# Optimization experiments

Hardware: AMD Instinct MI355X
Metric: run time of the kernel (lower is better)

The kernel has to match this reference:

```python
import jax, jax.numpy as jnp
import numpy as np

B, S, D, H = 8, 1024, 1024, 16
HD = D // H  # head_dim = 64
SCALE = HD ** -0.5


def setup_inputs() -> dict:
    key = jax.random.key(0)
    ks = jax.random.split(key, 10)
    std = D ** -0.5
    return {
        "hidden_states": jax.random.normal(ks[0], (B, S, D), jnp.float32),
        "attn_mask": jnp.zeros((B, 1, S, S), jnp.float32),
        "prev_attn_weights": jax.random.normal(ks[1], (B, H, S, S), jnp.float32),
        "Wq": jax.random.normal(ks[2], (D, D), jnp.float32) * std,
        "bq": jnp.zeros((D,), jnp.float32),
        "Wk": jax.random.normal(ks[3], (D, D), jnp.float32) * std,
        "bk": jnp.zeros((D,), jnp.float32),
        "Wv": jax.random.normal(ks[4], (D, D), jnp.float32) * std,
        "bv": jnp.zeros((D,), jnp.float32),
    }


def _split_heads(x):
    # (B, S, D) -> (B, H, S, HD)
    return x.reshape(B, S, H, HD).transpose(0, 2, 1, 3)


def reference(hidden_states, attn_mask, prev_attn_weights, Wq, bq, Wk, bk, Wv, bv):
    q = _split_heads(hidden_states @ Wq + bq)
    k = _split_heads(hidden_states @ Wk + bk)
    v = _split_heads(hidden_states @ Wv + bv)
    # scaled dot-product scores + additive mask + realformer residual scores
    scores = jnp.einsum("bhqd,bhkd->bhqk", q, k) * SCALE
    scores = scores + attn_mask + prev_attn_weights
    probs = jax.nn.softmax(scores, axis=-1)  # dropout p=0 (eval)
    ctx = jnp.einsum("bhqk,bhkd->bhqd", probs, v)
    # (B, H, S, HD) -> (B, S, D)
    out = ctx.transpose(0, 2, 1, 3).reshape(B, S, D)
    return out
```

## Files before the change

kernel.cpp:

```cpp
#include <hip/hip_runtime.h>

#define B_  8
#define S_  1024
#define D_  1024
#define H_  16
#define HD_ 64
#define M_  8192
#define LOG2E 1.44269504088896f
#define QSCALE_ (0.125f * 1.44269504088896f)
#define MSHIFT_ 20.0f

typedef __attribute__((ext_vector_type(8))) short bf16x8;
typedef __attribute__((ext_vector_type(4))) float f32x4;

__device__ __forceinline__ unsigned short f2b(float x) {
  union { float f; unsigned u; } un; un.f = x;
  unsigned r = un.u + 0x7FFFu + ((un.u >> 16) & 1u);
  return (unsigned short)(r >> 16);
}

__global__ __launch_bounds__(256) void k_convert_x(const float* __restrict__ x,
                                                   unsigned short* __restrict__ o) {
  int i = (blockIdx.x * 256 + threadIdx.x) * 4;
  const int n = M_ * D_;
  const int stride = gridDim.x * 256 * 4;
  for (; i < n; i += stride) {
    const float4 v = *(const float4*)(x + i);
    ushort4 r;
    r.x = f2b(v.x); r.y = f2b(v.y); r.z = f2b(v.z); r.w = f2b(v.w);
    *(ushort4*)(o + i) = r;
  }
}

__global__ __launch_bounds__(256) void k_transpose_w(const float* __restrict__ Wq,
    const float* __restrict__ Wk, const float* __restrict__ Wv,
    unsigned short* __restrict__ Wt) {
  __shared__ float t[64][65];
  const float* W = (blockIdx.z == 0) ? Wq : ((blockIdx.z == 1) ? Wk : Wv);
  unsigned short* dst = Wt + (size_t)blockIdx.z * (D_ * D_);
  const int k0 = blockIdx.x * 64, n0 = blockIdx.y * 64;
  const int tid = threadIdx.x;
#pragma unroll
  for (int i = 0; i < 16; ++i) {
    const int lin = i * 256 + tid;
    const int r = lin >> 6, c = lin & 63;
    t[r][c] = W[(size_t)(k0 + r) * D_ + n0 + c];
  }
  __syncthreads();
#pragma unroll
  for (int i = 0; i < 16; ++i) {
    const int lin = i * 256 + tid;
    const int r = lin >> 6, c = lin & 63;
    dst[(size_t)(n0 + r) * D_ + k0 + c] = f2b(t[c][r]);
  }
}

template <int MODE>
__global__ __launch_bounds__(256) void k_proj(const unsigned short* __restrict__ X,
    const unsigned short* __restrict__ Wt,
    const float* __restrict__ bq, const float* __restrict__ bk, const float* __restrict__ bv,
    unsigned short* __restrict__ Qw, unsigned short* __restrict__ Kw,
    unsigned short* __restrict__ Vt) {
  __shared__ unsigned short xs[128 * 32];
  __shared__ unsigned short wsh[128 * 32];
  const int tid = threadIdx.x;
  const int lane = tid & 63, wv = tid >> 6;
  const int g = lane >> 4, li = lane & 15;
  const int m0 = blockIdx.x * 128;
  const int n0 = blockIdx.y * 128;
  const int wr = wv >> 1, wc = wv & 1;
  const int wtrow0 = (MODE == 0) ? n0 : (2048 + n0);

  f32x4 acc[4][4];
#pragma unroll
  for (int i = 0; i < 4; ++i)
#pragma unroll
    for (int j = 0; j < 4; ++j) acc[i][j] = (f32x4){0.f, 0.f, 0.f, 0.f};

  const int srow = wv * 32 + (lane >> 2);
  const int skel = (lane & 3) * 8;

  for (int k0 = 0; k0 < D_; k0 += 32) {
#pragma unroll
    for (int i = 0; i < 2; ++i) {
      const unsigned short* gx = X + (size_t)(m0 + srow + i * 16) * D_ + k0 + skel;
      const unsigned short* gw = Wt + (size_t)(wtrow0 + srow + i * 16) * D_ + k0 + skel;
      __builtin_amdgcn_global_load_lds(
          (const __attribute__((address_space(1))) void*)gx,
          (__attribute__((address_space(3))) void*)&xs[(wv * 32 + i * 16) * 32], 16, 0, 0);
      __builtin_amdgcn_global_load_lds(
          (const __attribute__((address_space(1))) void*)gw,
          (__attribute__((address_space(3))) void*)&wsh[(wv * 32 + i * 16) * 32], 16, 0, 0);
    }
    __syncthreads();
    bf16x8 af[4], bfr[4];
#pragma unroll
    for (int i = 0; i < 4; ++i) {
      const int ar = wr * 64 + i * 16 + li;
      const int br = wc * 64 + i * 16 + li;
      if (MODE == 0) {
        af[i]  = *(const bf16x8*)&xs[ar * 32 + g * 8];
        bfr[i] = *(const bf16x8*)&wsh[br * 32 + g * 8];
      } else {
        af[i]  = *(const bf16x8*)&wsh[ar * 32 + g * 8];
        bfr[i] = *(const bf16x8*)&xs[br * 32 + g * 8];
      }
    }
#pragma unroll
    for (int i = 0; i < 4; ++i)
#pragma unroll
      for (int j = 0; j < 4; ++j)
        acc[i][j] = __builtin_amdgcn_mfma_f32_16x16x32_bf16(af[i], bfr[j], acc[i][j], 0, 0, 0);
    __syncthreads();
  }

  if (MODE == 0) {
#pragma unroll
    for (int j = 0; j < 4; ++j) {
      const int n = n0 + wc * 64 + j * 16 + li;
      const float bias = (n < D_) ? bq[n] : bk[n - D_];
#pragma unroll
      for (int i = 0; i < 4; ++i) {
#pragma unroll
        for (int r = 0; r < 4; ++r) {
          const int m = m0 + wr * 64 + i * 16 + g * 4 + r;
          const float v = acc[i][j][r] + bias;
          const int bb = m >> 10, ss = m & 1023;
          if (n < D_) {
            Qw[((size_t)(bb * H_ + (n >> 6)) * S_ + ss) * HD_ + (n & 63)] = f2b(v * QSCALE_);
          } else {
            const int nk = n - D_;
            Kw[((size_t)(bb * H_ + (nk >> 6)) * S_ + ss) * HD_ + (nk & 63)] = f2b(v);
          }
        }
      }
    }
  } else {
#pragma unroll
    for (int i = 0; i < 4; ++i) {
#pragma unroll
      for (int r = 0; r < 4; ++r) {
        const int nv = n0 + wr * 64 + i * 16 + g * 4 + r;
        const float bias = bv[nv];
#pragma unroll
        for (int j = 0; j < 4; ++j) {
          const int m = m0 + wc * 64 + j * 16 + li;
          const int bb = m >> 10, ss = m & 1023;
          const float v = acc[i][j][r] + bias;
          Vt[((size_t)(bb * H_ + (nv >> 6)) * HD_ + (nv & 63)) * S_ + ss] = f2b(v);
        }
      }
    }
  }
}

__global__ __launch_bounds__(256, 2) void k_attn(const unsigned short* __restrict__ Qw,
    const unsigned short* __restrict__ Kw, const unsigned short* __restrict__ Vt,
    const float* __restrict__ prev, const float* __restrict__ mask,
    float* __restrict__ out) {
  __shared__ unsigned short k_s[3][2048];
  __shared__ unsigned short v_s[3][2048];
  __shared__ float pm_s[3][4][2][64][4];
  __shared__ float mk_s[3][4][2][64][4];
  __shared__ unsigned short p_lds[4][16][40];
  const int tid = threadIdx.x;
  const int lane = tid & 63, wv = tid >> 6;
  const int g = lane >> 4, li = lane & 15;

  const int phys = blockIdx.x + 16 * blockIdx.y;
  const int xcd = phys & 7, idx = phys >> 3;
  const int qt = idx & 15;
  const int bh = xcd + 8 * (idx >> 4);
  const int b = bh >> 4, h = bh & 15;
  const int q0 = qt * 64 + wv * 16;

  const float* pdma = prev + (size_t)bh * S_ * S_ + (size_t)(q0 + li) * S_ + g * 4;
  const float* mdma = mask + (size_t)b * S_ * S_ + (size_t)(q0 + li) * S_ + g * 4;
  const unsigned short* kbase = Kw + (size_t)bh * S_ * HD_;
  const unsigned short* vbase = Vt + (size_t)bh * HD_ * S_;

  bf16x8 qf[2];
  {
    const unsigned short* qp = Qw + ((size_t)bh * S_ + q0 + li) * HD_ + g * 8;
    qf[0] = *(const bf16x8*)qp;
    qf[1] = *(const bf16x8*)(qp + 32);
  }

  const int krow = tid >> 3;
  const int kcol = (((tid & 7) ^ (krow & 7)) << 3);
  const int vrow = tid >> 2;
  const int vcol = ((tid & 3) << 3);

#define STAGE(TN, BI)                                                                      \
  {                                                                                        \
    const int sn = (TN) * 32;                                                              \
    __builtin_amdgcn_global_load_lds(                                                      \
        (const __attribute__((address_space(1))) void*)(kbase + (size_t)(sn + krow) * HD_ + kcol), \
        (__attribute__((address_space(3))) void*)(&k_s[BI][0] + wv * 512), 16, 0, 0);      \
    __builtin_amdgcn_global_load_lds(                                                      \
        (const __attribute__((address_space(1))) void*)(vbase + (size_t)vrow * S_ + sn + vcol), \
        (__attribute__((address_space(3))) void*)(&v_s[BI][0] + wv * 512), 16, 0, 0);      \
    __builtin_amdgcn_global_load_lds(                                                      \
        (const __attribute__((address_space(1))) void*)(pdma + sn),                        \
        (__attribute__((address_space(3))) void*)&pm_s[BI][wv][0][0][0], 16, 0, 0);        \
    __builtin_amdgcn_global_load_lds(                                                      \
        (const __attribute__((address_space(1))) void*)(pdma + sn + 16),                   \
        (__attribute__((address_space(3))) void*)&pm_s[BI][wv][1][0][0], 16, 0, 0);        \
    __builtin_amdgcn_global_load_lds(                                                      \
        (const __attribute__((address_space(1))) void*)(mdma + sn),                        \
        (__attribute__((address_space(3))) void*)&mk_s[BI][wv][0][0][0], 16, 0, 0);        \
    __builtin_amdgcn_global_load_lds(                                                      \
        (const __attribute__((address_space(1))) void*)(mdma + sn + 16),                   \
        (__attribute__((address_space(3))) void*)&mk_s[BI][wv][1][0][0], 16, 0, 0);        \
  }

  float lrun = 0.f;
  f32x4 ctx[4];
#pragma unroll
  for (int d = 0; d < 4; ++d) ctx[d] = (f32x4){0.f, 0.f, 0.f, 0.f};

  STAGE(0, 0);
  STAGE(1, 1);

#define PHASE(T, PB, NB, DOSTAGE, VM)                                                 \
  {                                                                                   \
    if (DOSTAGE) STAGE((T) + 2, NB);                                                  \
    asm volatile("s_waitcnt vmcnt(" #VM ")" ::: "memory");                            \
    __builtin_amdgcn_s_barrier();                                                     \
    {                                                                                 \
      const unsigned short* kb = &k_s[PB][0];                                         \
      const unsigned short* vb = &v_s[PB][0];                                         \
      f32x4 sa[2];                                                                    \
      __builtin_amdgcn_s_setprio(1);                                                  \
      _Pragma("unroll")                                                               \
      for (int cb = 0; cb < 2; ++cb) {                                                \
        const int r = cb * 16 + li;                                                   \
        const bf16x8 k0 = *(const bf16x8*)(kb + r * 64 + ((g ^ (r & 7)) << 3));       \
        const bf16x8 k1 = *(const bf16x8*)(kb + r * 64 + (((g + 4) ^ (r & 7)) << 3)); \
        f32x4 z = (f32x4){0.f, 0.f, 0.f, 0.f};                                        \
        z      = __builtin_amdgcn_mfma_f32_16x16x32_bf16(k0, qf[0], z, 0, 0, 0);      \
        sa[cb] = __builtin_amdgcn_mfma_f32_16x16x32_bf16(k1, qf[1], z, 0, 0, 0);      \
      }                                                                               \
      __builtin_amdgcn_s_setprio(0);                                                  \
      _Pragma("unroll")                                                               \
      for (int cb = 0; cb < 2; ++cb) {                                                \
        const f32x4 pv = *(const f32x4*)&pm_s[PB][wv][cb][lane][0];                   \
        const f32x4 mv = *(const f32x4*)&mk_s[PB][wv][cb][lane][0];                   \
        f32x4 pmc;                                                                    \
        pmc.x = fmaf(pv.x + mv.x, LOG2E, -MSHIFT_);                                   \
        pmc.y = fmaf(pv.y + mv.y, LOG2E, -MSHIFT_);                                   \
        pmc.z = fmaf(pv.z + mv.z, LOG2E, -MSHIFT_);                                   \
        pmc.w = fmaf(pv.w + mv.w, LOG2E, -MSHIFT_);                                   \
        const float e0 = exp2f(sa[cb][0] + pmc.x);                                    \
        const float e1 = exp2f(sa[cb][1] + pmc.y);                                    \
        const float e2 = exp2f(sa[cb][2] + pmc.z);                                    \
        const float e3 = exp2f(sa[cb][3] + pmc.w);                                    \
        lrun += (e0 + e1) + (e2 + e3);                                                \
        ushort4 pw;                                                                   \
        pw.x = f2b(e0); pw.y = f2b(e1); pw.z = f2b(e2); pw.w = f2b(e3);               \
        *(ushort4*)&p_lds[wv][li][cb * 16 + g * 4] = pw;                              \
      }                                                                               \
      const bf16x8 pf0 = *(const bf16x8*)&p_lds[wv][li][g * 8];                       \
      __builtin_amdgcn_s_setprio(1);                                                  \
      _Pragma("unroll")                                                               \
      for (int d = 0; d < 4; ++d) {                                                   \
        const bf16x8 v0 = *(const bf16x8*)(vb + (d * 16 + li) * 32 + g * 8);          \
        ctx[d] = __builtin_amdgcn_mfma_f32_16x16x32_bf16(pf0, v0, ctx[d], 0, 0, 0);   \
      }                                                                               \
      __builtin_amdgcn_s_setprio(0);                                                  \
    }                                                                                 \
    __builtin_amdgcn_s_barrier();                                                     \
  }

  for (int t = 0; t < 30; t += 3) {
    PHASE(t,     0, 2, 1, 12);
    PHASE(t + 1, 1, 0, 1, 12);
    PHASE(t + 2, 2, 1, 1, 12);
  }
  PHASE(30, 0, 2, 0, 6);
  PHASE(31, 1, 0, 0, 0);
#undef PHASE
#undef STAGE

  lrun += __shfl_xor(lrun, 16);
  lrun += __shfl_xor(lrun, 32);
#pragma unroll
  for (int j = 0; j < 4; ++j) {
    const float rs = __shfl(lrun, g * 4 + j);
    const float inv = 1.0f / rs;
    const int q = q0 + g * 4 + j;
    float* op = out + ((size_t)b * S_ + q) * D_ + h * HD_ + li;
#pragma unroll
    for (int d = 0; d < 4; ++d)
      op[d * 16] = ctx[d][j] * inv;
  }
}

extern "C" void kernel_launch(void* const* d_in, const int* in_sizes, int n_in,
                              void* d_out, int out_size, void* d_ws, size_t ws_size,
                              hipStream_t stream) {
  const float* hs   = (const float*)d_in[0];
  const float* mask = (const float*)d_in[1];
  const float* prev = (const float*)d_in[2];
  const float* Wq   = (const float*)d_in[3];
  const float* bq   = (const float*)d_in[4];
  const float* Wk   = (const float*)d_in[5];
  const float* bk   = (const float*)d_in[6];
  const float* Wv   = (const float*)d_in[7];
  const float* bv   = (const float*)d_in[8];
  float* out = (float*)d_out;

  char* ws = (char*)d_ws;
  unsigned short* Xbf = (unsigned short*)ws;
  unsigned short* Wt  = (unsigned short*)(ws + (16ull << 20));
  unsigned short* Qw  = (unsigned short*)(ws + (22ull << 20));
  unsigned short* Kw  = (unsigned short*)(ws + (38ull << 20));
  unsigned short* Vt  = (unsigned short*)(ws + (54ull << 20));

  k_convert_x<<<2048, 256, 0, stream>>>(hs, Xbf);
  k_transpose_w<<<dim3(16, 16, 3), 256, 0, stream>>>(Wq, Wk, Wv, Wt);
  k_proj<0><<<dim3(64, 16), 256, 0, stream>>>(Xbf, Wt, bq, bk, bv, Qw, Kw, Vt);
  k_proj<1><<<dim3(64, 8),  256, 0, stream>>>(Xbf, Wt, bq, bk, bv, Qw, Kw, Vt);
  k_attn<<<dim3(16, 128), 256, 0, stream>>>(Qw, Kw, Vt, prev, mask, out);
}
```

Measured before the change: 311.3 us.

## Double-buffer attention tiles and load mask into registers to raise occupancy

The attention kernel goes from triple- to double-buffered LDS staging for K, V and prev-scores. The mask tile is now prefetched one step ahead into registers instead of being DMA'd into LDS, and launch bounds rise from 2 to 4 blocks. This shrinks LDS per block so more blocks fit per CU, giving more concurrent waves to hide global-memory latency on the large prev-scores stream. In exchange, prefetch distance drops from two tiles to one, and the s_setprio hints around the MFMA sections are removed.

```diff
diff --git a/kernel.cpp b/kernel.cpp
--- a/kernel.cpp
+++ b/kernel.cpp
@@ -154,14 +154,13 @@
   }
 }
 
-__global__ __launch_bounds__(256, 2) void k_attn(const unsigned short* __restrict__ Qw,
+__global__ __launch_bounds__(256, 4) void k_attn(const unsigned short* __restrict__ Qw,
     const unsigned short* __restrict__ Kw, const unsigned short* __restrict__ Vt,
     const float* __restrict__ prev, const float* __restrict__ mask,
     float* __restrict__ out) {
-  __shared__ unsigned short k_s[3][2048];
-  __shared__ unsigned short v_s[3][2048];
-  __shared__ float pm_s[3][4][2][64][4];
-  __shared__ float mk_s[3][4][2][64][4];
+  __shared__ unsigned short k_s[2][2048];
+  __shared__ unsigned short v_s[2][2048];
+  __shared__ float pm_s[2][4][2][64][4];
   __shared__ unsigned short p_lds[4][16][40];
   const int tid = threadIdx.x;
   const int lane = tid & 63, wv = tid >> 6;
@@ -175,7 +174,7 @@
   const int q0 = qt * 64 + wv * 16;
 
   const float* pdma = prev + (size_t)bh * S_ * S_ + (size_t)(q0 + li) * S_ + g * 4;
-  const float* mdma = mask + (size_t)b * S_ * S_ + (size_t)(q0 + li) * S_ + g * 4;
+  const float* mb   = mask + (size_t)b * S_ * S_ + (size_t)(q0 + li) * S_ + g * 4;
   const unsigned short* kbase = Kw + (size_t)bh * S_ * HD_;
   const unsigned short* vbase = Vt + (size_t)bh * HD_ * S_;
 
@@ -187,18 +186,17 @@
   }
 
   const int krow = tid >> 3;
-  const int kcol = (((tid & 7) ^ (krow & 7)) << 3);
-  const int vrow = tid >> 2;
-  const int vcol = ((tid & 3) << 3);
+  const int koff = krow * HD_ + (((tid & 7) ^ (krow & 7)) << 3);
+  const int voff = (tid >> 2) * S_ + ((tid & 3) << 3);
 
 #define STAGE(TN, BI)                                                                      \
   {                                                                                        \
     const int sn = (TN) * 32;                                                              \
     __builtin_amdgcn_global_load_lds(                                                      \
-        (const __attribute__((address_space(1))) void*)(kbase + (size_t)(sn + krow) * HD_ + kcol), \
+        (const __attribute__((address_space(1))) void*)(kbase + (size_t)sn * HD_ + koff),  \
         (__attribute__((address_space(3))) void*)(&k_s[BI][0] + wv * 512), 16, 0, 0);      \
     __builtin_amdgcn_global_load_lds(                                                      \
-        (const __attribute__((address_space(1))) void*)(vbase + (size_t)vrow * S_ + sn + vcol), \
+        (const __attribute__((address_space(1))) void*)(vbase + voff + sn),                \
         (__attribute__((address_space(3))) void*)(&v_s[BI][0] + wv * 512), 16, 0, 0);      \
     __builtin_amdgcn_global_load_lds(                                                      \
         (const __attribute__((address_space(1))) void*)(pdma + sn),                        \
@@ -206,12 +204,6 @@
     __builtin_amdgcn_global_load_lds(                                                      \
         (const __attribute__((address_space(1))) void*)(pdma + sn + 16),                   \
         (__attribute__((address_space(3))) void*)&pm_s[BI][wv][1][0][0], 16, 0, 0);        \
-    __builtin_amdgcn_global_load_lds(                                                      \
-        (const __attribute__((address_space(1))) void*)(mdma + sn),                        \
-        (__attribute__((address_space(3))) void*)&mk_s[BI][wv][0][0][0], 16, 0, 0);        \
-    __builtin_amdgcn_global_load_lds(                                                      \
-        (const __attribute__((address_space(1))) void*)(mdma + sn + 16),                   \
-        (__attribute__((address_space(3))) void*)&mk_s[BI][wv][1][0][0], 16, 0, 0);        \
   }
 
   float lrun = 0.f;
@@ -219,38 +211,41 @@
 #pragma unroll
   for (int d = 0; d < 4; ++d) ctx[d] = (f32x4){0.f, 0.f, 0.f, 0.f};
 
+  f32x4 mA[2], mB[2];
+
   STAGE(0, 0);
-  STAGE(1, 1);
-
-#define PHASE(T, PB, NB, DOSTAGE, VM)                                                 \
+  mA[0] = *(const f32x4*)(mb);
+  mA[1] = *(const f32x4*)(mb + 16);
+
+#define PHASE(T, PB, NB, MCUR, MNXT)                                                  \
   {                                                                                   \
-    if (DOSTAGE) STAGE((T) + 2, NB);                                                  \
-    asm volatile("s_waitcnt vmcnt(" #VM ")" ::: "memory");                            \
+    const int tn = ((T) < 31) ? (T) + 1 : 31;                                         \
+    STAGE(tn, NB);                                                                    \
+    MNXT[0] = *(const f32x4*)(mb + tn * 32);                                          \
+    MNXT[1] = *(const f32x4*)(mb + tn * 32 + 16);                                     \
+    asm volatile("s_waitcnt vmcnt(6)" ::: "memory");                                  \
     __builtin_amdgcn_s_barrier();                                                     \
     {                                                                                 \
       const unsigned short* kb = &k_s[PB][0];                                         \
       const unsigned short* vb = &v_s[PB][0];                                         \
       f32x4 sa[2];                                                                    \
-      __builtin_amdgcn_s_setprio(1);                                                  \
       _Pragma("unroll")                                                               \
       for (int cb = 0; cb < 2; ++cb) {                                                \
         const int r = cb * 16 + li;                                                   \
-        const bf16x8 k0 = *(const bf16x8*)(kb + r * 64 + ((g ^ (r & 7)) << 3));       \
-        const bf16x8 k1 = *(const bf16x8*)(kb + r * 64 + (((g + 4) ^ (r & 7)) << 3)); \
+        const bf16x8 k0 = *(const bf16x8*)(kb + r * 64 + ((g ^ (li & 7)) << 3));      \
+        const bf16x8 k1 = *(const bf16x8*)(kb + r * 64 + (((4 + g) ^ (li & 7)) << 3)); \
         f32x4 z = (f32x4){0.f, 0.f, 0.f, 0.f};                                        \
         z      = __builtin_amdgcn_mfma_f32_16x16x32_bf16(k0, qf[0], z, 0, 0, 0);      \
         sa[cb] = __builtin_amdgcn_mfma_f32_16x16x32_bf16(k1, qf[1], z, 0, 0, 0);      \
       }                                                                               \
-      __builtin_amdgcn_s_setprio(0);                                                  \
       _Pragma("unroll")                                                               \
       for (int cb = 0; cb < 2; ++cb) {                                                \
         const f32x4 pv = *(const f32x4*)&pm_s[PB][wv][cb][lane][0];                   \
-        const f32x4 mv = *(const f32x4*)&mk_s[PB][wv][cb][lane][0];                   \
         f32x4 pmc;                                                                    \
-        pmc.x = fmaf(pv.x + mv.x, LOG2E, -MSHIFT_);                                   \
-        pmc.y = fmaf(pv.y + mv.y, LOG2E, -MSHIFT_);                                   \
-        pmc.z = fmaf(pv.z + mv.z, LOG2E, -MSHIFT_);                                   \
-        pmc.w = fmaf(pv.w + mv.w, LOG2E, -MSHIFT_);                                   \
+        pmc.x = fmaf(pv.x + MCUR[cb].x, LOG2E, -MSHIFT_);                             \
+        pmc.y = fmaf(pv.y + MCUR[cb].y, LOG2E, -MSHIFT_);                             \
+        pmc.z = fmaf(pv.z + MCUR[cb].z, LOG2E, -MSHIFT_);                             \
+        pmc.w = fmaf(pv.w + MCUR[cb].w, LOG2E, -MSHIFT_);                             \
         const float e0 = exp2f(sa[cb][0] + pmc.x);                                    \
         const float e1 = exp2f(sa[cb][1] + pmc.y);                                    \
         const float e2 = exp2f(sa[cb][2] + pmc.z);                                    \
@@ -260,27 +255,24 @@
         pw.x = f2b(e0); pw.y = f2b(e1); pw.z = f2b(e2); pw.w = f2b(e3);               \
         *(ushort4*)&p_lds[wv][li][cb * 16 + g * 4] = pw;                              \
       }                                                                               \
-      const bf16x8 pf0 = *(const bf16x8*)&p_lds[wv][li][g * 8];                       \
-      __builtin_amdgcn_s_setprio(1);                                                  \
+      const bf16x8 pf = *(const bf16x8*)&p_lds[wv][li][g * 8];                        \
       _Pragma("unroll")                                                               \
       for (int d = 0; d < 4; ++d) {                                                   \
-        const bf16x8 v0 = *(const bf16x8*)(vb + (d * 16 + li) * 32 + g * 8);          \
-        ctx[d] = __builtin_amdgcn_mfma_f32_16x16x32_bf16(pf0, v0, ctx[d], 0, 0, 0);   \
+        const bf16x8 vf = *(const bf16x8*)(vb + (d * 16 + li) * 32 + g * 8);          \
+        ctx[d] = __builtin_amdgcn_mfma_f32_16x16x32_bf16(pf, vf, ctx[d], 0, 0, 0);    \
       }                                                                               \
-      __builtin_amdgcn_s_setprio(0);                                                  \
     }                                                                                 \
     __builtin_amdgcn_s_barrier();                                                     \
   }
 
-  for (int t = 0; t < 30; t += 3) {
-    PHASE(t,     0, 2, 1, 12);
-    PHASE(t + 1, 1, 0, 1, 12);
-    PHASE(t + 2, 2, 1, 1, 12);
-  }
-  PHASE(30, 0, 2, 0, 6);
-  PHASE(31, 1, 0, 0, 0);
+  for (int t = 0; t < 32; t += 2) {
+    PHASE(t,     0, 1, mA, mB);
+    PHASE(t + 1, 1, 0, mB, mA);
+  }
 #undef PHASE
 #undef STAGE
+
+  asm volatile("s_waitcnt vmcnt(0)" ::: "memory");
 
   lrun += __shfl_xor(lrun, 16);
   lrun += __shfl_xor(lrun, 32);
```

Result: faster. 294.4 us (-5.4%).
